# Kernel tuning notes

Hardware: AMD Instinct MI355X
Metric: run time of the kernel (lower is better)

## Reference

```python
import jax, jax.numpy as jnp
import numpy as np


def _gcn_conv(x, W, b, src, dst, num_nodes):
    # PyG GCNConv: linear transform, add self-loops, symmetric normalization,
    # scatter-sum aggregation, then bias.
    h = x @ W  # [N, out]
    loop = jnp.arange(num_nodes, dtype=src.dtype)
    s = jnp.concatenate([src, loop])
    d = jnp.concatenate([dst, loop])
    deg = jax.ops.segment_sum(jnp.ones_like(s, dtype=h.dtype), d, num_segments=num_nodes)
    dinv = jnp.where(deg > 0, jax.lax.rsqrt(deg), 0.0)
    norm = dinv[s] * dinv[d]  # [E+N]
    msgs = h[s] * norm[:, None]  # gather + scale
    out = jax.ops.segment_sum(msgs, d, num_segments=num_nodes)
    return out + b


def setup_inputs() -> dict:
    key = jax.random.key(0)
    k1, k2, k3, k4 = jax.random.split(key, 4)
    N, F_in, H, C, E = 100000, 512, 16, 40, 3200000
    node_feature = jax.random.normal(k1, (N, F_in), dtype=jnp.float32)
    W1 = jax.random.normal(k2, (F_in, H), dtype=jnp.float32) * (1.0 / np.sqrt(F_in))
    b1 = jnp.zeros((H,), dtype=jnp.float32)
    W2 = jax.random.normal(k3, (H, C), dtype=jnp.float32) * (1.0 / np.sqrt(H))
    b2 = jnp.zeros((C,), dtype=jnp.float32)
    edge_index = jax.random.randint(k4, (2, E), 0, N, dtype=jnp.int64)
    return {"node_feature": node_feature, "W1": W1, "b1": b1,
            "W2": W2, "b2": b2, "edge_index": edge_index}


def reference(node_feature, W1, b1, W2, b2, edge_index):
    # Inference path: F.dropout(training=False) is identity.
    N = node_feature.shape[0]
    src, dst = edge_index[0], edge_index[1]
    x = jax.nn.elu(_gcn_conv(node_feature, W1, b1, src, dst, N))
    x = _gcn_conv(x, W2, b2, src, dst, N)
    return jax.nn.log_softmax(x, axis=1)
```

## Files before the change

kernel.cpp:

```cpp
#include <hip/hip_runtime.h>
#include <hip/hip_bf16.h>
#include <math.h>

__device__ __forceinline__ unsigned pk_bf16(float lo, float hi) {
    unsigned a = __float_as_uint(lo), b = __float_as_uint(hi);
    unsigned alo = (a + 0x7fffu + ((a >> 16) & 1u)) >> 16;
    unsigned bhi = (b + 0x7fffu + ((b >> 16) & 1u)) >> 16;
    return alo | (bhi << 16);
}
__device__ __forceinline__ float bf_lo(unsigned u) { return __uint_as_float(u << 16); }
__device__ __forceinline__ float bf_hi(unsigned u) { return __uint_as_float(u & 0xffff0000u); }


__global__ __launch_bounds__(256) void k_count(const int* __restrict__ dst,
                                               int* __restrict__ countsT,
                                               int E, int B, int NBLK, int CHUNK) {
    __shared__ int hist[1024];
    int tid = threadIdx.x, b = blockIdx.x;
    for (int j = tid; j < B; j += 256) hist[j] = 0;
    __syncthreads();
    int e0 = b * CHUNK, e1 = min(e0 + CHUNK, E);
    for (int i = e0 + tid * 4; i < e1; i += 1024) {
        if (i + 3 < e1) {
            int4 d4 = *(const int4*)(dst + i);
            atomicAdd(&hist[d4.x >> 7], 1);
            atomicAdd(&hist[d4.y >> 7], 1);
            atomicAdd(&hist[d4.z >> 7], 1);
            atomicAdd(&hist[d4.w >> 7], 1);
        } else {
            for (int k = i; k < e1; ++k) atomicAdd(&hist[dst[k] >> 7], 1);
        }
    }
    __syncthreads();
    for (int j = tid; j < B; j += 256) countsT[j * NBLK + b] = hist[j];
}

__global__ __launch_bounds__(256) void k_scanb(int* __restrict__ countsT,
                                               int* __restrict__ btotal, int NBLK) {
    __shared__ int sm[256];
    int j = blockIdx.x, tid = threadIdx.x;
    int v = (tid < NBLK) ? countsT[j * NBLK + tid] : 0;
    sm[tid] = v; __syncthreads();
    for (int off = 1; off < 256; off <<= 1) {
        int t = (tid >= off) ? sm[tid - off] : 0;
        __syncthreads(); sm[tid] += t; __syncthreads();
    }
    if (tid < NBLK) countsT[j * NBLK + tid] = sm[tid] - v;
    if (tid == 255) btotal[j] = sm[255];
}

__global__ __launch_bounds__(1024) void k_scanb2(const int* __restrict__ btotal,
                                                 int* __restrict__ bstart,
                                                 int* __restrict__ offs,
                                                 int B, int E, int N) {
    __shared__ int sm[1024];
    int tid = threadIdx.x;
    int v = (tid < B) ? btotal[tid] : 0;
    sm[tid] = v; __syncthreads();
    for (int off = 1; off < 1024; off <<= 1) {
        int t = (tid >= off) ? sm[tid - off] : 0;
        __syncthreads(); sm[tid] += t; __syncthreads();
    }
    if (tid < B) bstart[tid] = sm[tid] - v;
    if (tid == 0) { bstart[B] = E; offs[N] = E; }
}

__global__ __launch_bounds__(256) void k_place(const int* __restrict__ src,
                                               const int* __restrict__ dst,
                                               const int* __restrict__ countsT,
                                               const int* __restrict__ bstart,
                                               unsigned* __restrict__ ebuf,
                                               int E, int B, int NBLK, int CHUNK) {
    __shared__ int cur[1024];
    int tid = threadIdx.x, b = blockIdx.x;
    for (int j = tid; j < B; j += 256) cur[j] = bstart[j] + countsT[j * NBLK + b];
    __syncthreads();
    int e0 = b * CHUNK, e1 = min(e0 + CHUNK, E);
    for (int i = e0 + tid * 4; i < e1; i += 1024) {
        if (i + 3 < e1) {
            int4 d4 = *(const int4*)(dst + i);
            int4 s4 = *(const int4*)(src + i);
            int p0 = atomicAdd(&cur[d4.x >> 7], 1);
            int p1 = atomicAdd(&cur[d4.y >> 7], 1);
            int p2 = atomicAdd(&cur[d4.z >> 7], 1);
            int p3 = atomicAdd(&cur[d4.w >> 7], 1);
            ebuf[p0] = ((unsigned)(d4.x & 127) << 17) | (unsigned)s4.x;
            ebuf[p1] = ((unsigned)(d4.y & 127) << 17) | (unsigned)s4.y;
            ebuf[p2] = ((unsigned)(d4.z & 127) << 17) | (unsigned)s4.z;
            ebuf[p3] = ((unsigned)(d4.w & 127) << 17) | (unsigned)s4.w;
        } else {
            for (int k = i; k < e1; ++k) {
                int d = dst[k], s = src[k];
                int pos = atomicAdd(&cur[d >> 7], 1);
                ebuf[pos] = ((unsigned)(d & 127) << 17) | (unsigned)s;
            }
        }
    }
}

__global__ __launch_bounds__(256) void k_csr(const int* __restrict__ bstart,
                                             const unsigned* __restrict__ ebuf,
                                             int* __restrict__ csr,
                                             int* __restrict__ offs,
                                             float* __restrict__ dinv, int N) {
    __shared__ int sm[128];
    __shared__ int loc[128];
    int j = blockIdx.x, tid = threadIdx.x;
    int e0 = bstart[j], e1 = bstart[j + 1];
    if (tid < 128) sm[tid] = 0;
    __syncthreads();
    for (int i = e0 + tid; i < e1; i += 256) atomicAdd(&sm[ebuf[i] >> 17], 1);
    __syncthreads();
    int v = (tid < 128) ? sm[tid] : 0;
    for (int off = 1; off < 128; off <<= 1) {
        int t = (tid < 128 && tid >= off) ? sm[tid - off] : 0;
        __syncthreads();
        if (tid < 128) sm[tid] += t;
        __syncthreads();
    }
    if (tid < 128) {
        int ex = sm[tid] - v;
        loc[tid] = e0 + ex;
        int n = j * 128 + tid;
        if (n < N) {
            offs[n] = e0 + ex;
            dinv[n] = rsqrtf((float)v + 1.0f);
        }
    }
    __syncthreads();
    for (int i = e0 + tid; i < e1; i += 256) {
        unsigned eb = ebuf[i];
        int pos = atomicAdd(&loc[eb >> 17], 1);
        csr[pos] = (int)(eb & 0x1FFFFu);
    }
}

__global__ __launch_bounds__(256) void k_gemm1(
    const float* __restrict__ x, const float* __restrict__ W1,
    const float* __restrict__ dinv, unsigned* __restrict__ h1s, int N)
{
    __shared__ float4 lds4[4][128];
    const int lane = threadIdx.x & 63;
    const int wid  = threadIdx.x >> 6;
    const int g = lane >> 4, j = lane & 15;
    const int gwave  = blockIdx.x * 4 + wid;
    const int nwaves = gridDim.x * 4;

    float w[128];
    #pragma unroll
    for (int t = 0; t < 128; ++t) w[t] = W1[(g * 128 + t) * 16 + j];

    float* buf = (float*)lds4[wid];
    int row = gwave;
    if (row >= N) return;
    const float4* xr = (const float4*)(x + (size_t)row * 512);
    float4 a = xr[lane], b = xr[lane + 64];
    while (row < N) {
        int nrow = row + nwaves;
        float4 a2, b2;
        if (nrow < N) {
            const float4* xr2 = (const float4*)(x + (size_t)nrow * 512);
            a2 = xr2[lane]; b2 = xr2[lane + 64];
        }
        ((float4*)buf)[lane]      = a;
        ((float4*)buf)[lane + 64] = b;
        asm volatile("s_waitcnt lgkmcnt(0)" ::: "memory");
        const float4* bx = (const float4*)(buf + g * 128);
        float acc = 0.f;
        #pragma unroll
        for (int s = 0; s < 32; ++s) {
            float4 xv = bx[s];
            acc = fmaf(xv.x, w[4*s+0], acc);
            acc = fmaf(xv.y, w[4*s+1], acc);
            acc = fmaf(xv.z, w[4*s+2], acc);
            acc = fmaf(xv.w, w[4*s+3], acc);
        }
        acc += __shfl_xor(acc, 16);
        acc += __shfl_xor(acc, 32);
        float hv = 0.f;
        if (lane < 16) hv = acc * dinv[row];
        float oth = __shfl_xor(hv, 1);
        if (lane < 16 && !(lane & 1))
            h1s[(size_t)row * 8 + (j >> 1)] = pk_bf16(hv, oth);
        asm volatile("s_waitcnt lgkmcnt(0)" ::: "memory");
        row = nrow;
        a = a2; b = b2;
    }
}

__global__ __launch_bounds__(256) void k_l1(
    const int* __restrict__ offs, const int* __restrict__ csr,
    const unsigned* __restrict__ h1s, const float* __restrict__ dinv,
    const float* __restrict__ b1, unsigned* __restrict__ x1s, int N)
{
    const int lane = threadIdx.x & 63;
    const int wid  = threadIdx.x >> 6;
    const int gwave  = blockIdx.x * 4 + wid;
    const int nwaves = gridDim.x * 4;
    const int eg = lane >> 3, w = lane & 7;
    const float b1v = b1[lane & 15];

    for (int n = gwave; n < N; n += nwaves) {
        int o0 = offs[n], cnt = offs[n + 1] - o0;
        float accx = 0.f, accy = 0.f;
        for (int cb = 0; cb < cnt; cb += 64) {
            int cs = cnt - cb; if (cs > 64) cs = 64;
            int sreg = (lane < cs) ? csr[o0 + cb + lane] : 0;
            #pragma unroll
            for (int i = 0; i < 8; ++i) {
                int e = i * 8 + eg;
                int s = __shfl(sreg, e);
                if (e < cs) {
                    unsigned u = h1s[(size_t)s * 8 + w];
                    accx += bf_lo(u);
                    accy += bf_hi(u);
                }
            }
        }
        accx += __shfl_xor(accx, 8);  accy += __shfl_xor(accy, 8);
        accx += __shfl_xor(accx, 16); accy += __shfl_xor(accy, 16);
        accx += __shfl_xor(accx, 32); accy += __shfl_xor(accy, 32);

        float dv = dinv[n];
        float fx = __shfl(accx, lane >> 1), fy = __shfl(accy, lane >> 1);
        float xv = 0.f;
        if (lane < 16) {
            float aggv = (lane & 1) ? fy : fx;
            unsigned su = h1s[(size_t)n * 8 + (lane >> 1)];
            float self = (lane & 1) ? bf_hi(su) : bf_lo(su);
            xv = (aggv + self) * dv + b1v;
            xv = xv > 0.f ? xv : expm1f(xv);
            xv *= dv;
        }
        float oth = __shfl_xor(xv, 1);
        if (lane < 16 && !(lane & 1))
            x1s[(size_t)n * 8 + (lane >> 1)] = pk_bf16(xv, oth);
    }
}

__global__ __launch_bounds__(256) void k_l2(
    const int* __restrict__ offs, const int* __restrict__ csr,
    const unsigned* __restrict__ x1s, const float* __restrict__ dinv,
    const float* __restrict__ W2, const float* __restrict__ b2,
    float* __restrict__ out, int N)
{
    const int lane = threadIdx.x & 63;
    const int wid  = threadIdx.x >> 6;
    const int gwave  = blockIdx.x * 4 + wid;
    const int nwaves = gridDim.x * 4;
    const int eg = lane >> 3, w = lane & 7;
    const int c = lane < 40 ? lane : 39;

    float w2[16];
    #pragma unroll
    for (int t = 0; t < 16; ++t) w2[t] = W2[t * 40 + c];
    const float b2v = b2[c];

    for (int n = gwave; n < N; n += nwaves) {
        int o0 = offs[n], cnt = offs[n + 1] - o0;
        float accx = 0.f, accy = 0.f;
        for (int cb = 0; cb < cnt; cb += 64) {
            int cs = cnt - cb; if (cs > 64) cs = 64;
            int sreg = (lane < cs) ? csr[o0 + cb + lane] : 0;
            #pragma unroll
            for (int i = 0; i < 8; ++i) {
                int e = i * 8 + eg;
                int s = __shfl(sreg, e);
                if (e < cs) {
                    unsigned u = x1s[(size_t)s * 8 + w];
                    accx += bf_lo(u);
                    accy += bf_hi(u);
                }
            }
        }
        accx += __shfl_xor(accx, 8);  accy += __shfl_xor(accy, 8);
        accx += __shfl_xor(accx, 16); accy += __shfl_xor(accy, 16);
        accx += __shfl_xor(accx, 32); accy += __shfl_xor(accy, 32);

        float dv = dinv[n];
        float fx = __shfl(accx, lane >> 1), fy = __shfl(accy, lane >> 1);
        float xv = 0.f;
        if (lane < 16) {
            float aggv = (lane & 1) ? fy : fx;
            unsigned su = x1s[(size_t)n * 8 + (lane >> 1)];
            float self = (lane & 1) ? bf_hi(su) : bf_lo(su);
            xv = (aggv + self) * dv;
        }
        float v = b2v;
        #pragma unroll
        for (int t = 0; t < 16; ++t)
            v = fmaf(__shfl(xv, t), w2[t], v);

        float vm = (lane < 40) ? v : -INFINITY;
        #pragma unroll
        for (int off = 32; off; off >>= 1) vm = fmaxf(vm, __shfl_xor(vm, off));
        float ex = (lane < 40) ? expf(v - vm) : 0.f;
        float sum = ex;
        #pragma unroll
        for (int off = 32; off; off >>= 1) sum += __shfl_xor(sum, off);
        if (lane < 40) out[(size_t)n * 40 + lane] = v - vm - logf(sum);
    }
}

extern "C" void kernel_launch(void* const* d_in, const int* in_sizes, int n_in,
                              void* d_out, int out_size, void* d_ws, size_t ws_size,
                              hipStream_t stream) {
    const float* x  = (const float*)d_in[0];
    const float* W1 = (const float*)d_in[1];
    const float* b1 = (const float*)d_in[2];
    const float* W2 = (const float*)d_in[3];
    const float* b2 = (const float*)d_in[4];
    const int*   ei = (const int*)d_in[5];

    const int N = in_sizes[0] / 512;
    const int E = in_sizes[5] / 2;
    const int* src = ei;
    const int* dst = ei + E;

    const int B     = (N + 127) >> 7;
    const int CHUNK = 16384;
    const int NBLK  = (E + CHUNK - 1) / CHUNK;

    int*      countsT = (int*)d_ws;
    int*      btotal  = countsT + (size_t)B * NBLK;
    int*      bstart  = btotal + B;
    unsigned* ebuf    = (unsigned*)(bstart + B + 4);
    int*      csr     = (int*)(ebuf + E);
    int*      offs    = csr + E;
    float*    dinv    = (float*)(offs + N + 4);
    unsigned* h1s     = (unsigned*)(dinv + N);
    unsigned* x1s     = h1s + (size_t)8 * N;
    float*    out     = (float*)d_out;

    k_count <<<NBLK, 256, 0, stream>>>(dst, countsT, E, B, NBLK, CHUNK);
    k_scanb <<<B, 256, 0, stream>>>(countsT, btotal, NBLK);
    k_scanb2<<<1, 1024, 0, stream>>>(btotal, bstart, offs, B, E, N);
    k_place <<<NBLK, 256, 0, stream>>>(src, dst, countsT, bstart, ebuf, E, B, NBLK, CHUNK);
    k_csr   <<<B, 256, 0, stream>>>(bstart, ebuf, csr, offs, dinv, N);
    k_gemm1 <<<2048, 256, 0, stream>>>(x, W1, dinv, h1s, N);
    k_l1    <<<2048, 256, 0, stream>>>(offs, csr, h1s, dinv, b1, x1s, N);
    k_l2    <<<2048, 256, 0, stream>>>(offs, csr, x1s, dinv, W2, b2, out, N);
}
```

Measured before the change: 268.8 us.

## Compute first-layer GEMM with bf16 MFMA tiles instead of scalar FMAs

Rewrites the x·W1 kernel so each wave handles a 16-row tile with the 16x16x32 bf16 MFMA instruction. W1 fragments are preloaded into registers as packed bf16, and x is converted to bf16 on the fly, so the LDS staging and scalar FMA loop go away. The grid is halved to match the coarser per-wave work. This trades some input precision (x rounded to bf16) and a less contiguous per-lane load pattern for far fewer ALU instructions. It assumes N is a multiple of 16.

```diff
diff --git a/kernel.cpp b/kernel.cpp
--- a/kernel.cpp
+++ b/kernel.cpp
@@ -1,6 +1,9 @@
 #include <hip/hip_runtime.h>
 #include <hip/hip_bf16.h>
 #include <math.h>
+
+typedef __attribute__((ext_vector_type(8))) short bf16x8;
+typedef __attribute__((ext_vector_type(4))) float f32x4;
 
 __device__ __forceinline__ unsigned pk_bf16(float lo, float hi) {
     unsigned a = __float_as_uint(lo), b = __float_as_uint(hi);
@@ -139,52 +142,49 @@
     const float* __restrict__ x, const float* __restrict__ W1,
     const float* __restrict__ dinv, unsigned* __restrict__ h1s, int N)
 {
-    __shared__ float4 lds4[4][128];
     const int lane = threadIdx.x & 63;
     const int wid  = threadIdx.x >> 6;
-    const int g = lane >> 4, j = lane & 15;
     const int gwave  = blockIdx.x * 4 + wid;
     const int nwaves = gridDim.x * 4;
-
-    float w[128];
+    const int col = lane & 15;
+    const int kg  = lane >> 4;
+
+    unsigned bfr[16][4];
     #pragma unroll
-    for (int t = 0; t < 128; ++t) w[t] = W1[(g * 128 + t) * 16 + j];
-
-    float* buf = (float*)lds4[wid];
-    int row = gwave;
-    if (row >= N) return;
-    const float4* xr = (const float4*)(x + (size_t)row * 512);
-    float4 a = xr[lane], b = xr[lane + 64];
-    while (row < N) {
-        int nrow = row + nwaves;
-        float4 a2, b2;
-        if (nrow < N) {
-            const float4* xr2 = (const float4*)(x + (size_t)nrow * 512);
-            a2 = xr2[lane]; b2 = xr2[lane + 64];
-        }
-        ((float4*)buf)[lane]      = a;
-        ((float4*)buf)[lane + 64] = b;
-        asm volatile("s_waitcnt lgkmcnt(0)" ::: "memory");
-        const float4* bx = (const float4*)(buf + g * 128);
-        float acc = 0.f;
-        #pragma unroll
-        for (int s = 0; s < 32; ++s) {
-            float4 xv = bx[s];
-            acc = fmaf(xv.x, w[4*s+0], acc);
-            acc = fmaf(xv.y, w[4*s+1], acc);
-            acc = fmaf(xv.z, w[4*s+2], acc);
-            acc = fmaf(xv.w, w[4*s+3], acc);
-        }
-        acc += __shfl_xor(acc, 16);
-        acc += __shfl_xor(acc, 32);
-        float hv = 0.f;
-        if (lane < 16) hv = acc * dinv[row];
-        float oth = __shfl_xor(hv, 1);
-        if (lane < 16 && !(lane & 1))
-            h1s[(size_t)row * 8 + (j >> 1)] = pk_bf16(hv, oth);
-        asm volatile("s_waitcnt lgkmcnt(0)" ::: "memory");
-        row = nrow;
-        a = a2; b = b2;
+    for (int kk = 0; kk < 16; ++kk) {
+        int kbase = kk * 32 + kg * 8;
+        #pragma unroll
+        for (int i = 0; i < 4; ++i) {
+            float lo = W1[(size_t)(kbase + 2 * i) * 16 + col];
+            float hi = W1[(size_t)(kbase + 2 * i + 1) * 16 + col];
+            bfr[kk][i] = pk_bf16(lo, hi);
+        }
+    }
+
+    const int TT = N >> 4;
+    for (int t = gwave; t < TT; t += nwaves) {
+        const float* xr = x + (size_t)(t * 16 + col) * 512 + kg * 8;
+        f32x4 acc = {0.f, 0.f, 0.f, 0.f};
+        #pragma unroll
+        for (int kk = 0; kk < 16; ++kk) {
+            float4 xa = *(const float4*)(xr + kk * 32);
+            float4 xb = *(const float4*)(xr + kk * 32 + 4);
+            unsigned afr[4];
+            afr[0] = pk_bf16(xa.x, xa.y);
+            afr[1] = pk_bf16(xa.z, xa.w);
+            afr[2] = pk_bf16(xb.x, xb.y);
+            afr[3] = pk_bf16(xb.z, xb.w);
+            acc = __builtin_amdgcn_mfma_f32_16x16x32_bf16(
+                *(bf16x8*)afr, *(bf16x8*)&bfr[kk][0], acc, 0, 0, 0);
+        }
+        #pragma unroll
+        for (int m = 0; m < 4; ++m) {
+            int r = t * 16 + kg * 4 + m;
+            float v = acc[m] * dinv[r];
+            float oth = __shfl_xor(v, 1);
+            if (!(lane & 1))
+                h1s[(size_t)r * 8 + (col >> 1)] = pk_bf16(v, oth);
+        }
     }
 }
 
@@ -337,7 +337,7 @@
     k_scanb2<<<1, 1024, 0, stream>>>(btotal, bstart, offs, B, E, N);
     k_place <<<NBLK, 256, 0, stream>>>(src, dst, countsT, bstart, ebuf, E, B, NBLK, CHUNK);
     k_csr   <<<B, 256, 0, stream>>>(bstart, ebuf, csr, offs, dinv, N);
-    k_gemm1 <<<2048, 256, 0, stream>>>(x, W1, dinv, h1s, N);
+    k_gemm1 <<<1024, 256, 0, stream>>>(x, W1, dinv, h1s, N);
     k_l1    <<<2048, 256, 0, stream>>>(offs, csr, h1s, dinv, b1, x1s, N);
     k_l2    <<<2048, 256, 0, stream>>>(offs, csr, x1s, dinv, W2, b2, out, N);
 }
```

New measurement: 244.0 us. -9.2%, faster.
